# Kernel optimization log

Hardware: AMD Instinct MI355X
Metric: run time of the kernel (lower is better)

Reference implementation:

```python
import jax, jax.numpy as jnp
from jax import lax
import numpy as np

EPS = 1e-5

def _conv1x1(x, w, b=None):
    # x: [B,C,H,W], w: [O,C]
    y = jnp.einsum('oc,bchw->bohw', w, x)
    if b is not None:
        y = y + b[:, None, None]
    return y

def _bn(x, g, b, m, v):
    scale = g / jnp.sqrt(v + EPS)
    return (x - m[:, None, None]) * scale[:, None, None] + b[:, None, None]

def _conv_bn_silu(x, w, g, b, m, v):
    return jax.nn.silu(_bn(_conv1x1(x, w), g, b, m, v))

def _maxpool(x, k):
    p = k // 2
    return lax.reduce_window(x, -jnp.inf, lax.max, (1, 1, k, k), (1, 1, 1, 1),
                             ((0, 0), (0, 0), (p, p), (p, p)))

def _avgpool(x, k):
    # torch AvgPool2d default count_include_pad=True -> divide by k*k
    p = k // 2
    s = lax.reduce_window(x, 0.0, lax.add, (1, 1, k, k), (1, 1, 1, 1),
                          ((0, 0), (0, 0), (p, p), (p, p)))
    return s / float(k * k)

def setup_inputs() -> dict:
    key = jax.random.key(0)
    ks = jax.random.split(key, 18)
    f32 = jnp.float32
    B, C1, H, W = 8, 512, 64, 64
    c_ = C1 // 2          # 256
    C = c_ * 7            # 1792
    Cq = C // 8           # 224
    C2 = 512
    rn = lambda i, sh, s: jax.random.normal(ks[i], sh, dtype=f32) * s
    return {
        'x': rn(0, (B, C1, H, W), 1.0),
        'cv1_w': rn(1, (c_, C1), 0.05),
        'cv1_g': jax.random.uniform(ks[2], (c_,), dtype=f32),
        'cv1_b': rn(3, (c_,), 0.05),
        'cv1_m': jnp.zeros((c_,), f32),
        'cv1_v': jnp.ones((c_,), f32),
        'q_w': rn(4, (Cq, C), 0.02),
        'q_b': rn(5, (Cq,), 0.02),
        'k_w': rn(6, (Cq, C), 0.02),
        'k_b': rn(7, (Cq,), 0.02),
        'v_w': rn(8, (C, C), 0.02),
        'v_b': rn(9, (C,), 0.02),
        'gamma': rn(10, (1,), 0.5),
        'cv2_w': rn(11, (C2, C), 0.02),
        'cv2_g': jax.random.uniform(ks[12], (C2,), dtype=f32),
        'cv2_b': rn(13, (C2,), 0.05),
        'cv2_m': jnp.zeros((C2,), f32),
        'cv2_v': jnp.ones((C2,), f32),
    }

def _criss_cross(cat, q_w, q_b, k_w, k_b, v_w, v_b, gamma):
    B, C, H, W = cat.shape
    q = _conv1x1(cat, q_w, q_b)   # [B,Cq,H,W]
    k = _conv1x1(cat, k_w, k_b)
    v = _conv1x1(cat, v_w, v_b)   # [B,C,H,W]
    # column (H-axis) energies with -inf diagonal, row (W-axis) energies
    eH = jnp.einsum('bchw,bcgw->bhwg', q, k)        # [B,H,W,H]
    diag = jnp.eye(H, dtype=bool)[:, None, :]       # mask where h == g
    eH = jnp.where(diag, -jnp.inf, eH)
    eW = jnp.einsum('bchw,bchv->bhwv', q, k)        # [B,H,W,W]
    att = jax.nn.softmax(jnp.concatenate([eH, eW], axis=-1), axis=-1)
    attH, attW = att[..., :H], att[..., H:]
    outH = jnp.einsum('bcgw,bhwg->bchw', v, attH)
    outW = jnp.einsum('bchv,bhwv->bchw', v, attW)
    return gamma[0] * (outH + outW) + cat

def reference(x, cv1_w, cv1_g, cv1_b, cv1_m, cv1_v,
              q_w, q_b, k_w, k_b, v_w, v_b, gamma,
              cv2_w, cv2_g, cv2_b, cv2_m, cv2_v):
    x1 = _conv_bn_silu(x, cv1_w, cv1_g, cv1_b, cv1_m, cv1_v)   # [B,256,H,W]
    y1 = _maxpool(x1, 5)
    y2 = _maxpool(y1, 5)
    y3 = _maxpool(y2, 5)
    a1 = _avgpool(x1, 13)
    a2 = _avgpool(x1, 9)
    a3 = _avgpool(x1, 5)
    cat = jnp.concatenate([x1, y1, y2, y3, a1, a2, a3], axis=1)  # [B,1792,H,W]
    att = _criss_cross(cat, q_w, q_b, k_w, k_b, v_w, v_b, gamma)
    return _conv_bn_silu(att, cv2_w, cv2_g, cv2_b, cv2_m, cv2_v)
```

## Files before the change

### kernel.cpp

```cpp
#include <hip/hip_runtime.h>


typedef short bf16x8 __attribute__((ext_vector_type(8)));
typedef float f32x4  __attribute__((ext_vector_type(4)));

#define DEV __device__ __forceinline__

DEV float bf2f(unsigned short u) {
    unsigned int i = ((unsigned int)u) << 16;
    float f; __builtin_memcpy(&f, &i, 4); return f;
}
DEV unsigned short f2bf(float f) {
    unsigned int i; __builtin_memcpy(&i, &f, 4);
    unsigned int r = i + 0x7FFFu + ((i >> 16) & 1u);
    return (unsigned short)(r >> 16);
}
DEV float fsilu(float v) { return v / (1.f + __expf(-v)); }

#define GLL(gsrc, ldst)                                                        \
    __builtin_amdgcn_global_load_lds(                                          \
        (const __attribute__((address_space(1))) unsigned int*)(gsrc),         \
        (__attribute__((address_space(3))) unsigned int*)(ldst), 16, 0, 0)

#define MFMA(a, b, c) __builtin_amdgcn_mfma_f32_16x16x32_bf16((a), (b), (c), 0, 0, 0)

#define SBAR do {                                                              \
    __builtin_amdgcn_sched_barrier(0);                                         \
    __builtin_amdgcn_s_barrier();                                              \
    __builtin_amdgcn_sched_barrier(0); } while (0)
#define LGKM0 do {                                                             \
    asm volatile("s_waitcnt lgkmcnt(0)" ::: "memory");                         \
    __builtin_amdgcn_sched_barrier(0); } while (0)
#define VMC(n) do {                                                            \
    asm volatile("s_waitcnt vmcnt(" #n ")" ::: "memory");                      \
    __builtin_amdgcn_sched_barrier(0); } while (0)

__global__ __launch_bounds__(256) void prep_kernel(
    const float* __restrict__ cv1_w, const float* __restrict__ cv1_g,
    const float* __restrict__ cv1_b, const float* __restrict__ cv1_m,
    const float* __restrict__ cv1_v,
    const float* __restrict__ q_w, const float* __restrict__ q_b,
    const float* __restrict__ k_w, const float* __restrict__ k_b,
    const float* __restrict__ cv2_w,
    unsigned short* __restrict__ wb1, unsigned short* __restrict__ wqk,
    unsigned short* __restrict__ wc2,
    float* __restrict__ sc1, float* __restrict__ sh1,
    float* __restrict__ qkb, float* __restrict__ zeros)
{
    for (int i = blockIdx.x * 256 + threadIdx.x; i < 917504;
         i += gridDim.x * 256) {
        wc2[i] = f2bf(cv2_w[i]);
        int row = i / 1792;
        int col = i - row * 1792;
        float qv = (row < 224) ? q_w[i]
                   : (row < 448) ? k_w[(row - 224) * 1792 + col] : 0.f;
        wqk[i] = f2bf(qv);
        if (i < 131072) wb1[i] = f2bf(cv1_w[i]);
        if (i < 1792) zeros[i] = 0.f;
        if (i < 512) qkb[i] = (i < 224) ? q_b[i] : (i < 448 ? k_b[i - 224] : 0.f);
        if (i < 256) {
            float sc = cv1_g[i] * rsqrtf(cv1_v[i] + 1e-5f);
            sc1[i] = sc; sh1[i] = cv1_b[i] - cv1_m[i] * sc;
        }
    }
}

__global__ __launch_bounds__(256) void sh2_kernel(
    const float* __restrict__ cv2_w, const float* __restrict__ cv2_g,
    const float* __restrict__ cv2_b, const float* __restrict__ cv2_m,
    const float* __restrict__ cv2_v, const float* __restrict__ v_b,
    const float* __restrict__ gamma,
    float* __restrict__ sc2, float* __restrict__ sh2)
{
    const int i = blockIdx.x, tid = threadIdx.x;
    __shared__ float red[256];
    float s = 0.f;
    for (int k = tid; k < 1792; k += 256) s += cv2_w[i * 1792 + k] * v_b[k];
    red[tid] = s;
    __syncthreads();
#pragma unroll
    for (int off = 128; off > 0; off >>= 1) {
        if (tid < off) red[tid] += red[tid + off];
        __syncthreads();
    }
    if (tid == 0) {
        float sc = cv2_g[i] * rsqrtf(cv2_v[i] + 1e-5f);
        sc2[i] = sc;
        sh2[i] = cv2_b[i] - cv2_m[i] * sc + sc * gamma[0] * red[0];
    }
}

__global__ __launch_bounds__(256) void transpose_x(
    const float* __restrict__ x, unsigned short* __restrict__ xT)
{
    int bid = blockIdx.x;
    int nt = bid & 63, ct = (bid >> 6) & 7, b = bid >> 9;
    __shared__ float tile[64][65];
    int tid = threadIdx.x;
    int n0 = nt * 64, c0 = ct * 64;
#pragma unroll
    for (int it = 0; it < 16; ++it) {
        int idx = tid + it * 256;
        int r = idx >> 6, cc = idx & 63;
        tile[r][cc] = x[((long)(b * 512 + c0 + r)) * 4096 + n0 + cc];
    }
    __syncthreads();
#pragma unroll
    for (int it = 0; it < 16; ++it) {
        int idx = tid + it * 256;
        int r = idx >> 6, cc = idx & 63;
        xT[((long)(b * 4096 + n0 + r)) * 512 + c0 + cc] = f2bf(tile[cc][r]);
    }
}

__global__ __launch_bounds__(256) void transpose_w(
    const float* __restrict__ w, unsigned short* __restrict__ wT)
{
    int bid = blockIdx.x;
    int tx = bid % 28, ty = bid / 28;
    __shared__ float tile[64][65];
    int tid = threadIdx.x;
#pragma unroll
    for (int it = 0; it < 16; ++it) {
        int idx = tid + it * 256;
        int r = idx >> 6, cc = idx & 63;
        tile[r][cc] = w[((long)(ty * 64 + r)) * 1792 + tx * 64 + cc];
    }
    __syncthreads();
#pragma unroll
    for (int it = 0; it < 16; ++it) {
        int idx = tid + it * 256;
        int r = idx >> 6, cc = idx & 63;
        wT[((long)(tx * 64 + r)) * 1792 + ty * 64 + cc] = f2bf(tile[cc][r]);
    }
}

template <int EPI, bool DUAL>
__global__ __launch_bounds__(512, 2) void gemm256(
    const unsigned short* __restrict__ A, const unsigned short* __restrict__ B,
    const unsigned short* __restrict__ A2, const unsigned short* __restrict__ B2,
    int lda, int ldb, int K1, int K2,
    void* __restrict__ outp, int ldo,
    const float* __restrict__ p0, const float* __restrict__ p1)
{
    __shared__ __align__(16) unsigned short Ash[2][2][8192];
    __shared__ __align__(16) unsigned short Bsh[2][2][8192];
    const int tid = threadIdx.x, lane = tid & 63, wave = tid >> 6;
    const int wm = wave >> 2, wn = wave & 3;
    const long tile_m = (long)blockIdx.x * 256;
    const long tile_n = (long)blockIdx.y * 256;
    const int r0 = tid >> 2;
    const int ke0 = ((tid & 3) * 8) ^ (16 * ((r0 >> 3) & 1));
    const unsigned short* As0 = A + (tile_m + r0) * (long)lda + ke0;
    const unsigned short* As1 = A + (tile_m + r0 + 128) * (long)lda + ke0;
    const unsigned short* Bs0 = B + (tile_n + r0) * (long)ldb + ke0;
    const unsigned short* Bs1 = B + (tile_n + r0 + 128) * (long)ldb + ke0;
    const unsigned short* Cs0 = DUAL ? A2 + (tile_m + r0) * (long)lda + ke0 : As0;
    const unsigned short* Cs1 = DUAL ? A2 + (tile_m + r0 + 128) * (long)lda + ke0 : As1;
    const unsigned short* Ds0 = DUAL ? B2 + (tile_n + r0) * (long)ldb + ke0 : Bs0;
    const unsigned short* Ds1 = DUAL ? B2 + (tile_n + r0 + 128) * (long)ldb + ke0 : Bs1;
    const int dst0 = wave * 512;
    const int dst1 = 4096 + wave * 512;
    const int arow = lane & 15;
    const int kgs = ((lane >> 4) << 3) ^ (16 * ((arow >> 3) & 1));
    f32x4 acc[8][4] = {};
    bf16x8 a[8], b[4];
    const int nt1 = K1 >> 6;
    const int nt = nt1 + (DUAL ? (K2 >> 6) : 0);

#define PA0(t) ((DUAL && (t) >= nt1) ? Cs0 + (long)((t) - nt1) * 64 : As0 + (long)(t) * 64)
#define PA1(t) ((DUAL && (t) >= nt1) ? Cs1 + (long)((t) - nt1) * 64 : As1 + (long)(t) * 64)
#define PB0(t) ((DUAL && (t) >= nt1) ? Ds0 + (long)((t) - nt1) * 64 : Bs0 + (long)(t) * 64)
#define PB1(t) ((DUAL && (t) >= nt1) ? Ds1 + (long)((t) - nt1) * 64 : Bs1 + (long)(t) * 64)
#define STGA(db, kh, t) do {                                                   \
    GLL(PA0(t) + (kh) * 32, &Ash[db][kh][dst0]);                               \
    GLL(PA1(t) + (kh) * 32, &Ash[db][kh][dst1]); } while (0)
#define STGB(db, kh, t) do {                                                   \
    GLL(PB0(t) + (kh) * 32, &Bsh[db][kh][dst0]);                               \
    GLL(PB1(t) + (kh) * 32, &Bsh[db][kh][dst1]); } while (0)
#define LDA8(db, ks) do { _Pragma("unroll")                                    \
    for (int m = 0; m < 8; ++m)                                                \
        a[m] = *(const bf16x8*)&Ash[db][ks][(wm * 128 + m * 16 + arow) * 32 + kgs]; \
    } while (0)
#define LDB1(db, ks, n, slot)                                                  \
    b[slot] = *(const bf16x8*)&Bsh[db][ks][(wn * 64 + (n) * 16 + arow) * 32 + kgs]
#define MMA2(lo) do {                                                          \
    __builtin_amdgcn_s_setprio(1);                                             \
    _Pragma("unroll")                                                          \
    for (int m = 0; m < 8; ++m) {                                              \
        acc[m][lo]     = MFMA(a[m], b[lo],     acc[m][lo]);                    \
        acc[m][lo + 1] = MFMA(a[m], b[lo + 1], acc[m][lo + 1]);                \
    }                                                                          \
    __builtin_amdgcn_s_setprio(0); } while (0)

    STGA(0, 0, 0); STGB(0, 0, 0);
    STGA(0, 1, 0); STGB(0, 1, 0);
    {
        const int t1p = (1 < nt) ? 1 : 0;
        STGA(1, 0, t1p); STGB(1, 0, t1p);
    }
    VMC(4);
    SBAR;

    for (int kt = 0; kt < nt; ++kt) {
        const int db = kt & 1, sb = db ^ 1;
        const int t1c = (kt + 1 < nt) ? kt + 1 : nt - 1;
        const int t2c = (kt + 2 < nt) ? kt + 2 : nt - 1;
        LDA8(db, 0);
        LDB1(db, 0, 0, 0); LDB1(db, 0, 1, 1);
        STGA(sb, 1, t1c);
        LGKM0;
        MMA2(0);
        SBAR;
        LDB1(db, 0, 2, 2); LDB1(db, 0, 3, 3);
        STGB(sb, 1, t1c);
        LGKM0;
        MMA2(2);
        SBAR;
        LDA8(db, 1);
        LDB1(db, 1, 0, 0); LDB1(db, 1, 1, 1);
        STGA(db, 0, t2c);
        LGKM0;
        MMA2(0);
        SBAR;
        LDB1(db, 1, 2, 2); LDB1(db, 1, 3, 3);
        STGB(db, 0, t2c);
        LGKM0;
        MMA2(2);
        VMC(4);
        SBAR;
    }
    VMC(0);

    const int rbase = (lane >> 4) << 2;
#pragma unroll
    for (int n = 0; n < 4; ++n) {
        const int gcol = (int)tile_n + wn * 64 + n * 16 + arow;
        const float s0 = p0[gcol];
        const float s1 = (EPI != 1) ? p1[gcol] : 0.f;
#pragma unroll
        for (int m = 0; m < 8; ++m) {
            const long grow0 = tile_m + wm * 128 + m * 16 + rbase;
            if (EPI == 4) {
                const long bb = grow0 >> 12, pix = grow0 & 4095;
                float4 o4;
#pragma unroll
                for (int r = 0; r < 4; ++r) {
                    float v = acc[m][n][r] * s0 + s1;
                    ((float*)&o4)[r] = fsilu(v);
                }
                *(float4*)&((float*)outp)[((bb * 512 + gcol)) * 4096 + pix] = o4;
            } else {
#pragma unroll
                for (int r = 0; r < 4; ++r) {
                    float v = acc[m][n][r];
                    if (EPI != 1) { v = v * s0 + s1; v = fsilu(v); }
                    else          { v += s0; }
                    ((unsigned short*)outp)[(grow0 + r) * ldo + gcol] = f2bf(v);
                }
            }
        }
    }
#undef PA0
#undef PA1
#undef PB0
#undef PB1
#undef STGA
#undef STGB
#undef LDA8
#undef LDB1
#undef MMA2
}

template <int I>
DEV void pool_h_body(const unsigned short* x1s, unsigned short* pool,
                     int c, int w0, long obase)
{
    constexpr int R = 2 * (I + 1);
    constexpr int K = 2 * R + 1;
    unsigned short* qm = pool + (long)I * 32768 * 256;
    unsigned short* qs = pool + (long)(I + 3) * 32768 * 256;
    float pre[32];
    {
        float run = -1e30f;
        int ph = (w0 + 2 * R - (K - 1)) % K;
#pragma unroll
        for (int t = 0; t < 32 + K - 1; ++t) {
            int p = w0 + R - (K - 1) + t;
            if (ph == 0) run = -1e30f;
            float v = ((unsigned)p < 64u) ? bf2f(x1s[p * 256 + c]) : -1e30f;
            run = fmaxf(run, v);
            if (t >= K - 1) pre[t - (K - 1)] = run;
            ph = (ph + 1 == K) ? 0 : ph + 1;
        }
    }
    {
        float run = -1e30f;
        int ph = (w0 + 31 + (K - 1)) % K;
#pragma unroll
        for (int t = 0; t < 32 + K - 1; ++t) {
            int s = w0 + 31 - R + (K - 1) - t;
            if (ph == K - 1) run = -1e30f;
            float v = ((unsigned)s < 64u) ? bf2f(x1s[s * 256 + c]) : -1e30f;
            run = fmaxf(run, v);
            if (t >= K - 1) {
                int w = s + R;
                qm[obase + (long)w * 16384] =
                    f2bf(fmaxf(run, pre[31 + (K - 1) - t]));
            }
            ph = (ph == 0) ? K - 1 : ph - 1;
        }
    }
    {
        float s = 0.f;
        int lo0 = (w0 - R >= 0) ? w0 - R : 0;
        int hi0 = (w0 + R <= 63) ? w0 + R : 63;
        for (int d = lo0; d <= hi0; ++d) s += bf2f(x1s[d * 256 + c]);
        for (int ww = 0; ww < 32; ++ww) {
            int w = w0 + ww;
            qs[obase + (long)w * 16384] = f2bf(s);
            if (w + 1 + R <= 63) s += bf2f(x1s[(w + 1 + R) * 256 + c]);
            if (w - R >= 0)      s -= bf2f(x1s[(w - R) * 256 + c]);
        }
    }
}

__global__ __launch_bounds__(512) void pool_h_all(
    const unsigned short* __restrict__ catT, unsigned short* __restrict__ pool)
{
    const int b = blockIdx.x >> 6, h = blockIdx.x & 63;
    __shared__ __align__(16) unsigned short x1s[64 * 256];
    const int tid = threadIdx.x, lane = tid & 63, wave = tid >> 6;
    const long nb = (long)b * 4096 + h * 64;
#pragma unroll
    for (int j = 0; j < 4; ++j) {
        int chunk = j * 8 + wave;
        int o = chunk * 1024 + lane * 16;
        int e = o >> 1, w = e >> 8, c = e & 255;
        GLL(catT + (nb + w) * 1792 + c, (char*)x1s + chunk * 1024);
    }
    __syncthreads();
    const int c = tid & 255, wg = tid >> 8;
    const int w0 = wg * 32;
    const long obase = ((long)b * 4096 + h) * 256 + c;
    pool_h_body<0>(x1s, pool, c, w0, obase);
    pool_h_body<1>(x1s, pool, c, w0, obase);
    pool_h_body<2>(x1s, pool, c, w0, obase);
}

template <int I>
DEV void pool_v_body(const unsigned short* mslab, const unsigned short* sslab,
                     unsigned short* catT, int c, int h0, long dbase)
{
    constexpr int R = 2 * (I + 1);
    constexpr int K = 2 * R + 1;
    constexpr float SCL = (I == 0) ? (1.f / 25.f)
                        : (I == 1) ? (1.f / 81.f) : (1.f / 169.f);
    constexpr int MAXD = 256 * (I + 1);
    constexpr int SUMD = 1536 - 256 * I;
    float pre[32];
    {
        float run = -1e30f;
        int ph = (h0 + 2 * R - (K - 1)) % K;
#pragma unroll
        for (int t = 0; t < 32 + K - 1; ++t) {
            int p = h0 + R - (K - 1) + t;
            if (ph == 0) run = -1e30f;
            float v = ((unsigned)p < 64u) ? bf2f(mslab[p * 128 + c]) : -1e30f;
            run = fmaxf(run, v);
            if (t >= K - 1) pre[t - (K - 1)] = run;
            ph = (ph + 1 == K) ? 0 : ph + 1;
        }
    }
    {
        float run = -1e30f;
        int ph = (h0 + 31 + (K - 1)) % K;
#pragma unroll
        for (int t = 0; t < 32 + K - 1; ++t) {
            int s = h0 + 31 - R + (K - 1) - t;
            if (ph == K - 1) run = -1e30f;
            float v = ((unsigned)s < 64u) ? bf2f(mslab[s * 128 + c]) : -1e30f;
            run = fmaxf(run, v);
            if (t >= K - 1) {
                int h = s + R;
                catT[dbase + MAXD + (long)h * (64 * 1792)] =
                    f2bf(fmaxf(run, pre[31 + (K - 1) - t]));
            }
            ph = (ph == 0) ? K - 1 : ph - 1;
        }
    }
    {
        float s = 0.f;
        int lo0 = (h0 - R >= 0) ? h0 - R : 0;
        int hi0 = (h0 + R <= 63) ? h0 + R : 63;
        for (int d = lo0; d <= hi0; ++d) s += bf2f(sslab[d * 128 + c]);
        for (int hh = 0; hh < 32; ++hh) {
            int h = h0 + hh;
            catT[dbase + SUMD + (long)h * (64 * 1792)] = f2bf(s * SCL);
            if (h + 1 + R <= 63) s += bf2f(sslab[(h + 1 + R) * 128 + c]);
            if (h - R >= 0)      s -= bf2f(sslab[(h - R) * 128 + c]);
        }
    }
}

__global__ __launch_bounds__(256) void pool_v_all(
    const unsigned short* __restrict__ pool, unsigned short* __restrict__ catT)
{
    const int s6 = blockIdx.y;
    const int bid = blockIdx.x;
    const int chh = bid & 1, w = (bid >> 1) & 63, b = bid >> 7;
    const int c0 = chh * 128;
    __shared__ __align__(16) unsigned short mslab[64 * 128];
    __shared__ __align__(16) unsigned short sslab[64 * 128];
    const int tid = threadIdx.x, lane = tid & 63, wave = tid >> 6;
    const long sbase = ((long)b * 4096 + (long)w * 64) * 256 + c0;
    const unsigned short* msrc = pool + (long)s6 * 32768 * 256 + sbase;
    const unsigned short* ssrc = pool + (long)(s6 + 3) * 32768 * 256 + sbase;
#pragma unroll
    for (int j = 0; j < 4; ++j) {
        int o = j * 4096 + wave * 1024 + lane * 16;
        int hh = o >> 8, ce = (o & 255) >> 1;
        GLL(msrc + hh * 256 + ce, (char*)mslab + (j * 4096 + wave * 1024));
        GLL(ssrc + hh * 256 + ce, (char*)sslab + (j * 4096 + wave * 1024));
    }
    __syncthreads();
    const int c = tid & 127, hg = tid >> 7;
    const int h0 = hg * 32;
    const long dbase = ((long)b * 4096 + w) * 1792 + c0 + c;
    if (s6 == 0)      pool_v_body<0>(mslab, sslab, catT, c, h0, dbase);
    else if (s6 == 1) pool_v_body<1>(mslab, sslab, catT, c, h0, dbase);
    else              pool_v_body<2>(mslab, sslab, catT, c, h0, dbase);
}

__global__ __launch_bounds__(256) void scores_h(
    const unsigned short* __restrict__ qk, float* __restrict__ attHlog)
{
    const int b = blockIdx.x >> 6, w = blockIdx.x & 63;
    __shared__ __align__(16) unsigned short Qs[64 * 232];
    __shared__ __align__(16) unsigned short Ks[64 * 232];
    const int tid = threadIdx.x, lane = tid & 63, wave = tid >> 6;
#pragma unroll
    for (int j = 0; j < 14; ++j) {
        int idx = tid + j * 256;
        int s = idx >= 1792;
        int id2 = idx - s * 1792;
        int row = id2 / 28, cb = id2 - row * 28;
        bf16x8 v = *(const bf16x8*)(qk + ((long)b * 4096 + row * 64 + w) * 512 +
                                    s * 224 + cb * 8);
        *(bf16x8*)((s ? Ks : Qs) + row * 232 + cb * 8) = v;
    }
    __syncthreads();
    const int m0 = wave * 16, arow = lane & 15, kc = (lane >> 4) << 3;
    f32x4 acc[4] = {};
#pragma unroll
    for (int ks = 0; ks < 7; ++ks) {
        bf16x8 af = *(const bf16x8*)(Qs + (m0 + arow) * 232 + ks * 32 + kc);
#pragma unroll
        for (int nf = 0; nf < 4; ++nf) {
            bf16x8 bv = *(const bf16x8*)(Ks + (nf * 16 + arow) * 232 + ks * 32 + kc);
            acc[nf] = MFMA(af, bv, acc[nf]);
        }
    }
    const int rb = (lane >> 4) << 2;
#pragma unroll
    for (int nf = 0; nf < 4; ++nf) {
        int g = nf * 16 + arow;
#pragma unroll
        for (int r = 0; r < 4; ++r) {
            int h = m0 + rb + r;
            float v = acc[nf][r];
            if (g == h) v = -1e30f;
            attHlog[((long)(b * 64 + h) * 64 + w) * 64 + g] = v;
        }
    }
}

__global__ __launch_bounds__(256) void scores_w_softmax(
    const unsigned short* __restrict__ qk, const float* __restrict__ attHlog,
    unsigned short* __restrict__ att)
{
    const int b = blockIdx.x >> 6, h = blockIdx.x & 63;
    __shared__ __align__(16) unsigned short Qs[64 * 232];
    __shared__ __align__(16) unsigned short Ks[64 * 232];
    __shared__ float ews[64 * 65];
    const int tid = threadIdx.x, lane = tid & 63, wave = tid >> 6;
    const long nbase = (long)b * 4096 + h * 64;
#pragma unroll
    for (int j = 0; j < 14; ++j) {
        int idx = tid + j * 256;
        int s = idx >= 1792;
        int id2 = idx - s * 1792;
        int row = id2 / 28, cb = id2 - row * 28;
        bf16x8 v = *(const bf16x8*)(qk + (nbase + row) * 512 + s * 224 + cb * 8);
        *(bf16x8*)((s ? Ks : Qs) + row * 232 + cb * 8) = v;
    }
    __syncthreads();
    const int m0 = wave * 16, arow = lane & 15, kc = (lane >> 4) << 3;
    f32x4 acc[4] = {};
#pragma unroll
    for (int ks = 0; ks < 7; ++ks) {
        bf16x8 af = *(const bf16x8*)(Qs + (m0 + arow) * 232 + ks * 32 + kc);
#pragma unroll
        for (int nf = 0; nf < 4; ++nf) {
            bf16x8 bv = *(const bf16x8*)(Ks + (nf * 16 + arow) * 232 + ks * 32 + kc);
            acc[nf] = MFMA(af, bv, acc[nf]);
        }
    }
    const int rb = (lane >> 4) << 2;
#pragma unroll
    for (int nf = 0; nf < 4; ++nf)
#pragma unroll
        for (int r = 0; r < 4; ++r)
            ews[(m0 + rb + r) * 65 + nf * 16 + arow] = acc[nf][r];
    __syncthreads();
    const int wl = tid >> 2, p = tid & 3;
    float eh[16], ew[16];
    const float* hrow = attHlog + ((long)(b * 64 + h) * 64 + wl) * 64 + p * 16;
#pragma unroll
    for (int j = 0; j < 16; ++j) eh[j] = hrow[j];
#pragma unroll
    for (int j = 0; j < 16; ++j) ew[j] = ews[wl * 65 + p * 16 + j];
    float mx = -1e30f;
#pragma unroll
    for (int j = 0; j < 16; ++j) { mx = fmaxf(mx, eh[j]); mx = fmaxf(mx, ew[j]); }
    mx = fmaxf(mx, __shfl_xor(mx, 1));
    mx = fmaxf(mx, __shfl_xor(mx, 2));
    float sm = 0.f;
#pragma unroll
    for (int j = 0; j < 16; ++j) {
        eh[j] = __expf(eh[j] - mx); sm += eh[j];
        ew[j] = __expf(ew[j] - mx); sm += ew[j];
    }
    sm += __shfl_xor(sm, 1);
    sm += __shfl_xor(sm, 2);
    float inv = 1.f / sm;
    unsigned short* orow = att + ((long)(b * 64 + h) * 64 + wl) * 128;
#pragma unroll
    for (int j = 0; j < 16; ++j) orow[p * 16 + j] = f2bf(eh[j] * inv);
#pragma unroll
    for (int j = 0; j < 16; ++j) orow[64 + p * 16 + j] = f2bf(ew[j] * inv);
}

template <int MODE>
__global__ __launch_bounds__(256) void apply_att(
    const unsigned short* __restrict__ att, const unsigned short* __restrict__ vsrc,
    unsigned short* __restrict__ mixed, const float* __restrict__ gamma)
{
    const int ch = blockIdx.x & 3;
    const int i  = (blockIdx.x >> 2) & 63;
    const int b  = blockIdx.x >> 8;
    const int c0 = ch * 448;
    __shared__ __align__(16) unsigned short As[64 * 72];
    __shared__ __align__(16) unsigned short Vs[64 * 448];
    const int tid = threadIdx.x, lane = tid & 63, wave = tid >> 6;
#pragma unroll
    for (int j = 0; j < 2; ++j) {
        int idx = tid + j * 256;
        int hh = idx >> 3, cb = idx & 7;
        long pos = (MODE == 0) ? ((long)(b * 64 + hh) * 64 + i)
                               : ((long)(b * 64 + i) * 64 + hh);
        bf16x8 v = *(const bf16x8*)(att + pos * 128 + MODE * 64 + cb * 8);
        *(bf16x8*)(As + hh * 72 + cb * 8) = v;
    }
#pragma unroll
    for (int j = 0; j < 14; ++j) {
        int idx = tid + j * 256;
        int g = idx / 56, cb = idx - g * 56;
        long n = (MODE == 0) ? ((long)b * 4096 + g * 64 + i)
                             : ((long)b * 4096 + i * 64 + g);
        bf16x8 v = *(const bf16x8*)(vsrc + n * 1792 + c0 + cb * 8);
        int sw = (g >> 3) & 7;
        *(bf16x8*)(Vs + g * 448 + ((cb ^ sw) << 3)) = v;
    }
    __syncthreads();
    const int arow = lane & 15, kc8 = (lane >> 4) << 3;
    const int rb = (lane >> 4) << 2;
    f32x4 acc[4][7] = {};
#pragma unroll
    for (int ks = 0; ks < 2; ++ks) {
        const int k0 = ks * 32;
        bf16x8 af[4];
#pragma unroll
        for (int m = 0; m < 4; ++m)
            af[m] = *(const bf16x8*)(As + (m * 16 + arow) * 72 + k0 + kc8);
        const int g0 = k0 + kc8;
        const int sw = (g0 >> 3) & 7;
#pragma unroll
        for (int nf = 0; nf < 7; ++nf) {
            int cl = wave * 112 + nf * 16 + arow;
            int cb = cl >> 3, clo = cl & 7;
            const unsigned short* pp = Vs + g0 * 448 + ((cb ^ sw) << 3) + clo;
            bf16x8 bv;
#pragma unroll
            for (int j = 0; j < 8; ++j) bv[j] = (short)pp[j * 448];
#pragma unroll
            for (int m = 0; m < 4; ++m)
                acc[m][nf] = MFMA(af[m], bv, acc[m][nf]);
        }
    }
    const float gam = gamma[0];
#pragma unroll
    for (int nf = 0; nf < 7; ++nf) {
        const int c = c0 + wave * 112 + nf * 16 + arow;
#pragma unroll
        for (int m = 0; m < 4; ++m) {
#pragma unroll
            for (int r = 0; r < 4; ++r) {
                const int rl = m * 16 + rb + r;
                long n = (MODE == 0) ? ((long)b * 4096 + rl * 64 + i)
                                     : ((long)b * 4096 + i * 64 + rl);
                long idx2 = n * 1792 + c;
                if (MODE == 0) {
                    mixed[idx2] = f2bf(acc[m][nf][r]);
                } else {
                    float pv = bf2f(mixed[idx2]);
                    mixed[idx2] = f2bf(gam * (acc[m][nf][r] + pv));
                }
            }
        }
    }
}

extern "C" void kernel_launch(void* const* d_in, const int* in_sizes, int n_in,
                              void* d_out, int out_size, void* d_ws, size_t ws_size,
                              hipStream_t stream)
{
    const float* x     = (const float*)d_in[0];
    const float* cv1_w = (const float*)d_in[1];
    const float* cv1_g = (const float*)d_in[2];
    const float* cv1_b = (const float*)d_in[3];
    const float* cv1_m = (const float*)d_in[4];
    const float* cv1_v = (const float*)d_in[5];
    const float* q_w   = (const float*)d_in[6];
    const float* q_b   = (const float*)d_in[7];
    const float* k_w   = (const float*)d_in[8];
    const float* k_b   = (const float*)d_in[9];
    const float* v_w   = (const float*)d_in[10];
    const float* v_b   = (const float*)d_in[11];
    const float* gamma = (const float*)d_in[12];
    const float* cv2_w = (const float*)d_in[13];
    const float* cv2_g = (const float*)d_in[14];
    const float* cv2_b = (const float*)d_in[15];
    const float* cv2_m = (const float*)d_in[16];
    const float* cv2_v = (const float*)d_in[17];

    char* ws = (char*)d_ws;
    unsigned short* wb1  = (unsigned short*)(ws + 0);
    unsigned short* wqk  = (unsigned short*)(ws + 262144);
    unsigned short* wc2  = (unsigned short*)(ws + 2097152);
    unsigned short* w2g  = (unsigned short*)(ws + 3932160);
    float* sc1           = (float*)(ws + 5767168);
    float* sh1           = (float*)(ws + 5775360);
    float* sc2           = (float*)(ws + 5783552);
    float* sh2           = (float*)(ws + 5791744);
    float* qkb           = (float*)(ws + 5799936);
    float* zeros         = (float*)(ws + 5808128);
    unsigned short* catT = (unsigned short*)(ws + 6291456);
    const long C_OFF = 123731968;
    unsigned short* xT    = (unsigned short*)(ws + C_OFF);
    unsigned short* wvT   = (unsigned short*)(ws + C_OFF + 33554432);
    unsigned short* poolb = (unsigned short*)(ws + C_OFF);
    unsigned short* mixed = (unsigned short*)(ws + C_OFF);
    unsigned short* qk    = (unsigned short*)d_out;
    float* attHlog        = (float*)((char*)d_out + 33554432);
    unsigned short* attb  = (unsigned short*)((char*)d_out + 41943040);

    prep_kernel<<<1024, 256, 0, stream>>>(
        cv1_w, cv1_g, cv1_b, cv1_m, cv1_v, q_w, q_b, k_w, k_b, cv2_w,
        wb1, wqk, wc2, sc1, sh1, qkb, zeros);

    sh2_kernel<<<512, 256, 0, stream>>>(
        cv2_w, cv2_g, cv2_b, cv2_m, cv2_v, v_b, gamma, sc2, sh2);

    transpose_x<<<4096, 256, 0, stream>>>(x, xT);
    transpose_w<<<784, 256, 0, stream>>>(v_w, wvT);

    gemm256<1, false><<<dim3(2, 7), 512, 0, stream>>>(
        wc2, wvT, wc2, wvT, 1792, 1792, 1792, 0, w2g, 1792, zeros, nullptr);

    gemm256<0, false><<<dim3(128, 1), 512, 0, stream>>>(
        xT, wb1, xT, wb1, 512, 512, 512, 0, catT, 1792, sc1, sh1);

    pool_h_all<<<512, 512, 0, stream>>>(catT, poolb);
    pool_v_all<<<dim3(1024, 3), 256, 0, stream>>>(poolb, catT);

    gemm256<1, false><<<dim3(128, 2), 512, 0, stream>>>(
        catT, wqk, catT, wqk, 1792, 1792, 1792, 0, qk, 512, qkb, nullptr);

    scores_h<<<512, 256, 0, stream>>>(qk, attHlog);
    scores_w_softmax<<<512, 256, 0, stream>>>(qk, attHlog, attb);

    apply_att<0><<<2048, 256, 0, stream>>>(attb, catT, mixed, gamma);
    apply_att<1><<<2048, 256, 0, stream>>>(attb, catT, mixed, gamma);

    gemm256<4, true><<<dim3(128, 2), 512, 0, stream>>>(
        mixed, w2g, catT, wc2, 1792, 1792, 1792, 1792, d_out, 0, sc2, sh2);
}
```

Measured before the change: 563.1 us.

## Merge prep kernels and small GEMMs into fewer launches; XCD-aware block mapping

Folds the four preprocessing kernels (weight casts, BN scale/shift, x and v_w transposes) into one launch with block-range dispatch. It also merges the w2g GEMM and the cv1 GEMM into one launch. The later GEMMs switch to a 1D grid that maps consecutive blocks onto the same XCD so the two N-tiles of one M-tile share L2. The aim is to cut launch and tail overhead and improve cache locality, but it gives up any ordering or concurrency tuning between the merged parts.

```diff
diff --git a/kernel.cpp b/kernel.cpp
--- a/kernel.cpp
+++ b/kernel.cpp
@@ -35,120 +35,20 @@
     asm volatile("s_waitcnt vmcnt(" #n ")" ::: "memory");                      \
     __builtin_amdgcn_sched_barrier(0); } while (0)
 
-__global__ __launch_bounds__(256) void prep_kernel(
-    const float* __restrict__ cv1_w, const float* __restrict__ cv1_g,
-    const float* __restrict__ cv1_b, const float* __restrict__ cv1_m,
-    const float* __restrict__ cv1_v,
-    const float* __restrict__ q_w, const float* __restrict__ q_b,
-    const float* __restrict__ k_w, const float* __restrict__ k_b,
-    const float* __restrict__ cv2_w,
-    unsigned short* __restrict__ wb1, unsigned short* __restrict__ wqk,
-    unsigned short* __restrict__ wc2,
-    float* __restrict__ sc1, float* __restrict__ sh1,
-    float* __restrict__ qkb, float* __restrict__ zeros)
-{
-    for (int i = blockIdx.x * 256 + threadIdx.x; i < 917504;
-         i += gridDim.x * 256) {
-        wc2[i] = f2bf(cv2_w[i]);
-        int row = i / 1792;
-        int col = i - row * 1792;
-        float qv = (row < 224) ? q_w[i]
-                   : (row < 448) ? k_w[(row - 224) * 1792 + col] : 0.f;
-        wqk[i] = f2bf(qv);
-        if (i < 131072) wb1[i] = f2bf(cv1_w[i]);
-        if (i < 1792) zeros[i] = 0.f;
-        if (i < 512) qkb[i] = (i < 224) ? q_b[i] : (i < 448 ? k_b[i - 224] : 0.f);
-        if (i < 256) {
-            float sc = cv1_g[i] * rsqrtf(cv1_v[i] + 1e-5f);
-            sc1[i] = sc; sh1[i] = cv1_b[i] - cv1_m[i] * sc;
-        }
-    }
-}
-
-__global__ __launch_bounds__(256) void sh2_kernel(
-    const float* __restrict__ cv2_w, const float* __restrict__ cv2_g,
-    const float* __restrict__ cv2_b, const float* __restrict__ cv2_m,
-    const float* __restrict__ cv2_v, const float* __restrict__ v_b,
-    const float* __restrict__ gamma,
-    float* __restrict__ sc2, float* __restrict__ sh2)
-{
-    const int i = blockIdx.x, tid = threadIdx.x;
-    __shared__ float red[256];
-    float s = 0.f;
-    for (int k = tid; k < 1792; k += 256) s += cv2_w[i * 1792 + k] * v_b[k];
-    red[tid] = s;
-    __syncthreads();
-#pragma unroll
-    for (int off = 128; off > 0; off >>= 1) {
-        if (tid < off) red[tid] += red[tid + off];
-        __syncthreads();
-    }
-    if (tid == 0) {
-        float sc = cv2_g[i] * rsqrtf(cv2_v[i] + 1e-5f);
-        sc2[i] = sc;
-        sh2[i] = cv2_b[i] - cv2_m[i] * sc + sc * gamma[0] * red[0];
-    }
-}
-
-__global__ __launch_bounds__(256) void transpose_x(
-    const float* __restrict__ x, unsigned short* __restrict__ xT)
-{
-    int bid = blockIdx.x;
-    int nt = bid & 63, ct = (bid >> 6) & 7, b = bid >> 9;
-    __shared__ float tile[64][65];
-    int tid = threadIdx.x;
-    int n0 = nt * 64, c0 = ct * 64;
-#pragma unroll
-    for (int it = 0; it < 16; ++it) {
-        int idx = tid + it * 256;
-        int r = idx >> 6, cc = idx & 63;
-        tile[r][cc] = x[((long)(b * 512 + c0 + r)) * 4096 + n0 + cc];
-    }
-    __syncthreads();
-#pragma unroll
-    for (int it = 0; it < 16; ++it) {
-        int idx = tid + it * 256;
-        int r = idx >> 6, cc = idx & 63;
-        xT[((long)(b * 4096 + n0 + r)) * 512 + c0 + cc] = f2bf(tile[cc][r]);
-    }
-}
-
-__global__ __launch_bounds__(256) void transpose_w(
-    const float* __restrict__ w, unsigned short* __restrict__ wT)
-{
-    int bid = blockIdx.x;
-    int tx = bid % 28, ty = bid / 28;
-    __shared__ float tile[64][65];
-    int tid = threadIdx.x;
-#pragma unroll
-    for (int it = 0; it < 16; ++it) {
-        int idx = tid + it * 256;
-        int r = idx >> 6, cc = idx & 63;
-        tile[r][cc] = w[((long)(ty * 64 + r)) * 1792 + tx * 64 + cc];
-    }
-    __syncthreads();
-#pragma unroll
-    for (int it = 0; it < 16; ++it) {
-        int idx = tid + it * 256;
-        int r = idx >> 6, cc = idx & 63;
-        wT[((long)(tx * 64 + r)) * 1792 + ty * 64 + cc] = f2bf(tile[cc][r]);
-    }
-}
-
 template <int EPI, bool DUAL>
-__global__ __launch_bounds__(512, 2) void gemm256(
+DEV void gemm_core(
+    unsigned short (&Ash)[2][2][8192], unsigned short (&Bsh)[2][2][8192],
+    int bx, int by,
     const unsigned short* __restrict__ A, const unsigned short* __restrict__ B,
     const unsigned short* __restrict__ A2, const unsigned short* __restrict__ B2,
     int lda, int ldb, int K1, int K2,
     void* __restrict__ outp, int ldo,
     const float* __restrict__ p0, const float* __restrict__ p1)
 {
-    __shared__ __align__(16) unsigned short Ash[2][2][8192];
-    __shared__ __align__(16) unsigned short Bsh[2][2][8192];
     const int tid = threadIdx.x, lane = tid & 63, wave = tid >> 6;
     const int wm = wave >> 2, wn = wave & 3;
-    const long tile_m = (long)blockIdx.x * 256;
-    const long tile_n = (long)blockIdx.y * 256;
+    const long tile_m = (long)bx * 256;
+    const long tile_n = (long)by * 256;
     const int r0 = tid >> 2;
     const int ke0 = ((tid & 3) * 8) ^ (16 * ((r0 >> 3) & 1));
     const unsigned short* As0 = A + (tile_m + r0) * (long)lda + ke0;
@@ -272,6 +172,133 @@
 #undef MMA2
 }
 
+template <int EPI, bool DUAL>
+__global__ __launch_bounds__(512, 2) void gemm_pair(
+    const unsigned short* __restrict__ A, const unsigned short* __restrict__ B,
+    const unsigned short* __restrict__ A2, const unsigned short* __restrict__ B2,
+    int lda, int ldb, int K1, int K2,
+    void* __restrict__ outp, int ldo,
+    const float* __restrict__ p0, const float* __restrict__ p1)
+{
+    __shared__ __align__(16) unsigned short Ash[2][2][8192];
+    __shared__ __align__(16) unsigned short Bsh[2][2][8192];
+    const int bid = blockIdx.x;
+    const int xcd = bid & 7, idx = bid >> 3;
+    const int m = xcd + 8 * (idx >> 1);
+    const int n = idx & 1;
+    gemm_core<EPI, DUAL>(Ash, Bsh, m, n, A, B, A2, B2, lda, ldb, K1, K2,
+                         outp, ldo, p0, p1);
+}
+
+__global__ __launch_bounds__(512, 2) void gemm_wcv1(
+    const unsigned short* __restrict__ wc2, const unsigned short* __restrict__ wvT,
+    unsigned short* __restrict__ w2g, const float* __restrict__ zeros,
+    const unsigned short* __restrict__ xT, const unsigned short* __restrict__ wb1,
+    unsigned short* __restrict__ catT,
+    const float* __restrict__ sc1, const float* __restrict__ sh1)
+{
+    __shared__ __align__(16) unsigned short Ash[2][2][8192];
+    __shared__ __align__(16) unsigned short Bsh[2][2][8192];
+    const int bid = blockIdx.x;
+    if (bid < 14) {
+        const int bx = bid / 7, by = bid % 7;
+        gemm_core<1, false>(Ash, Bsh, bx, by, wc2, wvT, wc2, wvT,
+                            1792, 1792, 1792, 0, w2g, 1792, zeros, nullptr);
+    } else {
+        const int bx = bid - 14;
+        gemm_core<0, false>(Ash, Bsh, bx, 0, xT, wb1, xT, wb1,
+                            512, 512, 512, 0, catT, 1792, sc1, sh1);
+    }
+}
+
+__global__ __launch_bounds__(256) void prep_all(
+    const float* __restrict__ x, unsigned short* __restrict__ xT,
+    const float* __restrict__ v_w, unsigned short* __restrict__ wvT,
+    const float* __restrict__ cv1_w, const float* __restrict__ cv1_g,
+    const float* __restrict__ cv1_b, const float* __restrict__ cv1_m,
+    const float* __restrict__ cv1_v,
+    const float* __restrict__ q_w, const float* __restrict__ q_b,
+    const float* __restrict__ k_w, const float* __restrict__ k_b,
+    const float* __restrict__ cv2_w,
+    unsigned short* __restrict__ wb1, unsigned short* __restrict__ wqk,
+    unsigned short* __restrict__ wc2,
+    float* __restrict__ sc1, float* __restrict__ sh1,
+    float* __restrict__ qkb, float* __restrict__ zeros,
+    const float* __restrict__ cv2_g, const float* __restrict__ cv2_b,
+    const float* __restrict__ cv2_m, const float* __restrict__ cv2_v,
+    const float* __restrict__ v_b, const float* __restrict__ gamma,
+    float* __restrict__ sc2, float* __restrict__ sh2)
+{
+    const int bid = blockIdx.x, tid = threadIdx.x;
+    __shared__ __align__(16) float tile[64][65];
+    if (bid < 4096) {
+        int nt = bid & 63, ct = (bid >> 6) & 7, b = bid >> 9;
+        int n0 = nt * 64, c0 = ct * 64;
+#pragma unroll
+        for (int it = 0; it < 16; ++it) {
+            int idx = tid + it * 256;
+            int r = idx >> 6, cc = idx & 63;
+            tile[r][cc] = x[((long)(b * 512 + c0 + r)) * 4096 + n0 + cc];
+        }
+        __syncthreads();
+#pragma unroll
+        for (int it = 0; it < 16; ++it) {
+            int idx = tid + it * 256;
+            int r = idx >> 6, cc = idx & 63;
+            xT[((long)(b * 4096 + n0 + r)) * 512 + c0 + cc] = f2bf(tile[cc][r]);
+        }
+    } else if (bid < 4880) {
+        int id = bid - 4096;
+        int tx = id % 28, ty = id / 28;
+#pragma unroll
+        for (int it = 0; it < 16; ++it) {
+            int idx = tid + it * 256;
+            int r = idx >> 6, cc = idx & 63;
+            tile[r][cc] = v_w[((long)(ty * 64 + r)) * 1792 + tx * 64 + cc];
+        }
+        __syncthreads();
+#pragma unroll
+        for (int it = 0; it < 16; ++it) {
+            int idx = tid + it * 256;
+            int r = idx >> 6, cc = idx & 63;
+            wvT[((long)(tx * 64 + r)) * 1792 + ty * 64 + cc] = f2bf(tile[cc][r]);
+        }
+    } else if (bid < 5904) {
+        for (int i = (bid - 4880) * 256 + tid; i < 917504; i += 1024 * 256) {
+            wc2[i] = f2bf(cv2_w[i]);
+            int row = i / 1792;
+            int col = i - row * 1792;
+            float qv = (row < 224) ? q_w[i]
+                       : (row < 448) ? k_w[(row - 224) * 1792 + col] : 0.f;
+            wqk[i] = f2bf(qv);
+            if (i < 131072) wb1[i] = f2bf(cv1_w[i]);
+            if (i < 1792) zeros[i] = 0.f;
+            if (i < 512) qkb[i] = (i < 224) ? q_b[i] : (i < 448 ? k_b[i - 224] : 0.f);
+            if (i < 256) {
+                float sc = cv1_g[i] * rsqrtf(cv1_v[i] + 1e-5f);
+                sc1[i] = sc; sh1[i] = cv1_b[i] - cv1_m[i] * sc;
+            }
+        }
+    } else {
+        const int i = bid - 5904;
+        float* red = &tile[0][0];
+        float s = 0.f;
+        for (int k = tid; k < 1792; k += 256) s += cv2_w[i * 1792 + k] * v_b[k];
+        red[tid] = s;
+        __syncthreads();
+#pragma unroll
+        for (int off = 128; off > 0; off >>= 1) {
+            if (tid < off) red[tid] += red[tid + off];
+            __syncthreads();
+        }
+        if (tid == 0) {
+            float sc = cv2_g[i] * rsqrtf(cv2_v[i] + 1e-5f);
+            sc2[i] = sc;
+            sh2[i] = cv2_b[i] - cv2_m[i] * sc + sc * gamma[0] * red[0];
+        }
+    }
+}
+
 template <int I>
 DEV void pool_h_body(const unsigned short* x1s, unsigned short* pool,
                      int c, int w0, long obase)
@@ -665,26 +692,19 @@
     float* attHlog        = (float*)((char*)d_out + 33554432);
     unsigned short* attb  = (unsigned short*)((char*)d_out + 41943040);
 
-    prep_kernel<<<1024, 256, 0, stream>>>(
+    prep_all<<<6416, 256, 0, stream>>>(
+        x, xT, v_w, wvT,
         cv1_w, cv1_g, cv1_b, cv1_m, cv1_v, q_w, q_b, k_w, k_b, cv2_w,
-        wb1, wqk, wc2, sc1, sh1, qkb, zeros);
-
-    sh2_kernel<<<512, 256, 0, stream>>>(
-        cv2_w, cv2_g, cv2_b, cv2_m, cv2_v, v_b, gamma, sc2, sh2);
-
-    transpose_x<<<4096, 256, 0, stream>>>(x, xT);
-    transpose_w<<<784, 256, 0, stream>>>(v_w, wvT);
-
-    gemm256<1, false><<<dim3(2, 7), 512, 0, stream>>>(
-        wc2, wvT, wc2, wvT, 1792, 1792, 1792, 0, w2g, 1792, zeros, nullptr);
-
-    gemm256<0, false><<<dim3(128, 1), 512, 0, stream>>>(
-        xT, wb1, xT, wb1, 512, 512, 512, 0, catT, 1792, sc1, sh1);
+        wb1, wqk, wc2, sc1, sh1, qkb, zeros,
+        cv2_g, cv2_b, cv2_m, cv2_v, v_b, gamma, sc2, sh2);
+
+    gemm_wcv1<<<142, 512, 0, stream>>>(wc2, wvT, w2g, zeros,
+                                       xT, wb1, catT, sc1, sh1);
 
     pool_h_all<<<512, 512, 0, stream>>>(catT, poolb);
     pool_v_all<<<dim3(1024, 3), 256, 0, stream>>>(poolb, catT);
 
-    gemm256<1, false><<<dim3(128, 2), 512, 0, stream>>>(
+    gemm_pair<1, false><<<256, 512, 0, stream>>>(
         catT, wqk, catT, wqk, 1792, 1792, 1792, 0, qk, 512, qkb, nullptr);
 
     scores_h<<<512, 256, 0, stream>>>(qk, attHlog);
@@ -693,6 +713,6 @@
     apply_att<0><<<2048, 256, 0, stream>>>(attb, catT, mixed, gamma);
     apply_att<1><<<2048, 256, 0, stream>>>(attb, catT, mixed, gamma);
 
-    gemm256<4, true><<<dim3(128, 2), 512, 0, stream>>>(
+    gemm_pair<4, true><<<256, 512, 0, stream>>>(
         mixed, w2g, catT, wc2, 1792, 1792, 1792, 1792, d_out, 0, sc2, sh2);
 }
```

After: 513.1 us, median of 3. 8.9% less time.
